# Kernel tuning notes

Hardware: AMD Instinct MI355X
Metric: run time of the kernel (lower is better)

Reference implementation:

```python
import jax, jax.numpy as jnp
import numpy as np

NUM_HEADS = 8
IN_CH = 512
SCALING = float(IN_CH // 8) ** (-0.5)  # 0.125, as in the torch module


def _conv1x1(x, w, b):
    # x: [B,C,H,W], w: [O,C], b: [O]  (1x1 conv == channel matmul)
    return jnp.einsum('bchw,oc->bohw', x, w) + b[None, :, None, None]


def setup_inputs() -> dict:
    key = jax.random.key(0)
    ks = jax.random.split(key, 9)
    B, C, H, W = 4, IN_CH, 96, 96
    q = jax.random.normal(ks[0], (B, C, H, W), jnp.float32)
    v = jax.random.normal(ks[1], (B, C, H, W), jnp.float32)
    # xavier_uniform for [C,C] 1x1 conv weights
    limit = float(np.sqrt(6.0 / (C + C)))
    Wq = jax.random.uniform(ks[2], (C, C), jnp.float32, -limit, limit)
    Wk = jax.random.uniform(ks[3], (C, C), jnp.float32, -limit, limit)
    Wv = jax.random.uniform(ks[4], (C, C), jnp.float32, -limit, limit)
    bq = jnp.zeros((C,), jnp.float32)
    bk = jnp.zeros((C,), jnp.float32)
    bv = jnp.zeros((C,), jnp.float32)
    # gamma is init to 0 in the module; use a nonzero value so the output is nontrivial
    gamma = jax.random.normal(ks[5], (1,), jnp.float32) * 0.1
    return {'q': q, 'v': v, 'Wq': Wq, 'bq': bq, 'Wk': Wk, 'bk': bk,
            'Wv': Wv, 'bv': bv, 'gamma': gamma}


def reference(q, v, Wq, bq, Wk, bk, Wv, bv, gamma):
    B, C, H, W = q.shape
    nh = NUM_HEADS
    hd = C // nh
    t = _conv1x1(q, Wq, bq) * SCALING           # proj_query
    f = _conv1x1(q, Wk, bk)                     # proj_key
    g = _conv1x1(v, Wv, bv)                     # proj_value
    t = t.reshape(B * nh, hd, H, W)
    f = f.reshape(B * nh, hd, H, W)
    g = g.reshape(B * nh, hd, H, W)
    # criss-cross affinity: row (same y, all x') and column (same x, all y'!=y)
    e_row = jnp.einsum('bdyx,bdyi->byxi', t, f)  # [Bh, H, W, W]
    e_col = jnp.einsum('bdyx,bdix->byxi', t, f)  # [Bh, H, W, H]
    # exclude the current position from the column branch (CUDA kernel skips i==y)
    diag = (jnp.arange(H)[:, None, None] == jnp.arange(H)[None, None, :])  # [H,1,H]
    e_col = jnp.where(diag, -jnp.inf, e_col)
    attn = jax.nn.softmax(jnp.concatenate([e_row, e_col], axis=-1), axis=-1)  # [Bh,H,W,W+H]
    a_row, a_col = attn[..., :W], attn[..., W:]
    out = (jnp.einsum('byxi,bdyi->bdyx', a_row, g)
           + jnp.einsum('byxi,bdix->bdyx', a_col, g))  # [Bh, hd, H, W]
    out = out.reshape(B, C, H, W)
    return gamma[0] * out + v
```

## Files before the change

kernel.cpp:

```cpp
#include <hip/hip_runtime.h>
#include <hip/hip_bf16.h>

typedef __bf16 bf16;
typedef __attribute__((ext_vector_type(8))) __bf16 bf16x8;
typedef __attribute__((ext_vector_type(4))) float floatx4;

#define B_  4
#define C_  512
#define H_  96
#define W_  96
#define HD_ 64
#define HW_ 9216
#define BH_ 32
#define SCALING_ 0.125f
#define BHS_ 589824

static constexpr size_t T_ELEMS = (size_t)BH_ * HD_ * HW_;
static constexpr size_t S_ELEMS = (size_t)BH_ * HW_;

__global__ __launch_bounds__(256) void cast_w(
    const float* __restrict__ Wq, const float* __restrict__ Wk, const float* __restrict__ Wv,
    bf16* __restrict__ Wb)
{
    const int i  = blockIdx.x * 256 + threadIdx.x;
    const int e0 = i * 4;
    const int arr = e0 >> 18;
    const int off = e0 & 262143;
    const float* W = (arr == 0) ? Wq : (arr == 1) ? Wk : Wv;
    const float4 val = *(const float4*)(W + off);
    bf16 tmp[4] __attribute__((aligned(8)));
    tmp[0] = (bf16)val.x; tmp[1] = (bf16)val.y; tmp[2] = (bf16)val.z; tmp[3] = (bf16)val.w;
    *(uint2*)(Wb + e0) = *(const uint2*)tmp;
}

__global__ __launch_bounds__(256) void cast_qv(
    const float* __restrict__ q, const float* __restrict__ v,
    bf16* __restrict__ qbT, bf16* __restrict__ vbT)
{
    const int z = blockIdx.z;
    const int s = z >> 2, b = z & 3;
    const float* sb = (s ? v : q) + (size_t)b * C_ * HW_;
    bf16*       db = (s ? vbT : qbT) + (size_t)b * HW_ * C_;
    const int p0 = blockIdx.x * 64, c0 = blockIdx.y * 64;

    __shared__ float ts[64][65];
    const int tid = threadIdx.x;

    for (int i = tid; i < 1024; i += 256) {
        const int row = i >> 4, seg = i & 15;
        const float4 val = *(const float4*)(sb + (size_t)(c0 + row) * HW_ + p0 + seg * 4);
        ts[row][seg * 4 + 0] = val.x; ts[row][seg * 4 + 1] = val.y;
        ts[row][seg * 4 + 2] = val.z; ts[row][seg * 4 + 3] = val.w;
    }
    __syncthreads();
    for (int i = tid; i < 512; i += 256) {
        const int prow = i >> 3, cseg = i & 7;
        bf16 tmp[8] __attribute__((aligned(16)));
        #pragma unroll
        for (int k = 0; k < 8; k++) tmp[k] = (bf16)ts[cseg * 8 + k][prow];
        *(uint4*)(db + (size_t)(p0 + prow) * C_ + c0 + cseg * 8) = *(const uint4*)tmp;
    }
}

__device__ __forceinline__ void stage_swz(
    const bf16* __restrict__ A, const bf16* __restrict__ Bsrc,
    int o0, int p0, int k0, int tid, bf16* As, bf16* Bs)
{
    #pragma unroll
    for (int c = tid; c < 512; c += 256) {
        const int sc = c ^ ((c >> 3) & 7);
        const int row = sc >> 2, seg = sc & 3;
        const bf16* gA = A    + (size_t)(o0 + row) * C_ + k0 + seg * 8;
        const bf16* gB = Bsrc + (size_t)(p0 + row) * C_ + k0 + seg * 8;
#if __has_builtin(__builtin_amdgcn_global_load_lds)
        char* lA = (char*)As + (size_t)(c & ~63) * 16;
        char* lB = (char*)Bs + (size_t)(c & ~63) * 16;
        __builtin_amdgcn_global_load_lds((const __attribute__((address_space(1))) void*)gA,
                                         (__attribute__((address_space(3))) void*)lA, 16, 0, 0);
        __builtin_amdgcn_global_load_lds((const __attribute__((address_space(1))) void*)gB,
                                         (__attribute__((address_space(3))) void*)lB, 16, 0, 0);
#else
        *(uint4*)((char*)As + (size_t)c * 16) = *(const uint4*)gA;
        *(uint4*)((char*)Bs + (size_t)c * 16) = *(const uint4*)gB;
#endif
    }
}

__device__ __forceinline__ void stage3_swz(
    const bf16* __restrict__ A0, const bf16* __restrict__ A1, const bf16* __restrict__ Bsrc,
    int o0, int p0, int k0, int tid, bf16* As0, bf16* As1, bf16* Bs)
{
    #pragma unroll
    for (int c = tid; c < 512; c += 256) {
        const int sc = c ^ ((c >> 3) & 7);
        const int row = sc >> 2, seg = sc & 3;
        const bf16* gA0 = A0   + (size_t)(o0 + row) * C_ + k0 + seg * 8;
        const bf16* gA1 = A1   + (size_t)(o0 + row) * C_ + k0 + seg * 8;
        const bf16* gB  = Bsrc + (size_t)(p0 + row) * C_ + k0 + seg * 8;
#if __has_builtin(__builtin_amdgcn_global_load_lds)
        char* lA0 = (char*)As0 + (size_t)(c & ~63) * 16;
        char* lA1 = (char*)As1 + (size_t)(c & ~63) * 16;
        char* lB  = (char*)Bs  + (size_t)(c & ~63) * 16;
        __builtin_amdgcn_global_load_lds((const __attribute__((address_space(1))) void*)gA0,
                                         (__attribute__((address_space(3))) void*)lA0, 16, 0, 0);
        __builtin_amdgcn_global_load_lds((const __attribute__((address_space(1))) void*)gA1,
                                         (__attribute__((address_space(3))) void*)lA1, 16, 0, 0);
        __builtin_amdgcn_global_load_lds((const __attribute__((address_space(1))) void*)gB,
                                         (__attribute__((address_space(3))) void*)lB, 16, 0, 0);
#else
        *(uint4*)((char*)As0 + (size_t)c * 16) = *(const uint4*)gA0;
        *(uint4*)((char*)As1 + (size_t)c * 16) = *(const uint4*)gA1;
        *(uint4*)((char*)Bs  + (size_t)c * 16) = *(const uint4*)gB;
#endif
    }
}

__device__ __forceinline__ int swz_chunk(int r, int quad)
{
    return (r * 4 + quad) ^ ((r >> 1) & 7);
}

__device__ __forceinline__ void compute_swz(
    const bf16* As, const bf16* Bs,
    int mrow, int ncol, int l16, int quad, floatx4 acc[4][4])
{
    bf16x8 af[4], bf_[4];
    #pragma unroll
    for (int i = 0; i < 4; i++)
        af[i] = *(const bf16x8*)&As[swz_chunk(mrow + i * 16 + l16, quad) * 8];
    #pragma unroll
    for (int j = 0; j < 4; j++)
        bf_[j] = *(const bf16x8*)&Bs[swz_chunk(ncol + j * 16 + l16, quad) * 8];
    #pragma unroll
    for (int i = 0; i < 4; i++)
        #pragma unroll
        for (int j = 0; j < 4; j++)
            acc[i][j] = __builtin_amdgcn_mfma_f32_16x16x32_bf16(af[i], bf_[j], acc[i][j], 0, 0, 0);
}

__device__ __forceinline__ void compute2_swz(
    const bf16* As0, const bf16* As1, const bf16* Bs,
    int mrow, int ncol, int l16, int quad, floatx4 acc0[4][4], floatx4 acc1[4][4])
{
    bf16x8 a0[4], a1[4], bb[4];
    #pragma unroll
    for (int i = 0; i < 4; i++) {
        const int pc = swz_chunk(mrow + i * 16 + l16, quad);
        a0[i] = *(const bf16x8*)&As0[pc * 8];
        a1[i] = *(const bf16x8*)&As1[pc * 8];
    }
    #pragma unroll
    for (int j = 0; j < 4; j++)
        bb[j] = *(const bf16x8*)&Bs[swz_chunk(ncol + j * 16 + l16, quad) * 8];
    #pragma unroll
    for (int i = 0; i < 4; i++)
        #pragma unroll
        for (int j = 0; j < 4; j++)
            acc0[i][j] = __builtin_amdgcn_mfma_f32_16x16x32_bf16(a0[i], bb[j], acc0[i][j], 0, 0, 0);
    #pragma unroll
    for (int i = 0; i < 4; i++)
        #pragma unroll
        for (int j = 0; j < 4; j++)
            acc1[i][j] = __builtin_amdgcn_mfma_f32_16x16x32_bf16(a1[i], bb[j], acc1[i][j], 0, 0, 0);
}

__global__ __launch_bounds__(256, 2) void conv_qk(
    const bf16* __restrict__ Wb,
    const float* __restrict__ bq, const float* __restrict__ bk,
    const bf16* __restrict__ qbT,
    bf16* __restrict__ tR, bf16* __restrict__ fR)
{
    const int b = blockIdx.z;
    const bf16* A0   = Wb;
    const bf16* A1   = Wb + (size_t)C_ * C_;
    const bf16* Bsrc = qbT + (size_t)b * HW_ * C_;

    const int p0 = blockIdx.x * 128;
    const int o0 = blockIdx.y * 128;

    __shared__ __align__(16) bf16 smem[24576];
    bf16* const As0_0 = smem;
    bf16* const As1_0 = smem + 4096;
    bf16* const Bs_0  = smem + 8192;
    bf16* const As0_1 = smem + 12288;
    bf16* const As1_1 = smem + 16384;
    bf16* const Bs_1  = smem + 20480;

    const int tid = threadIdx.x, lane = tid & 63;
    const int wave = tid >> 6, l16 = lane & 15, quad = lane >> 4;
    const int mrow = (wave >> 1) * 64, ncol = (wave & 1) * 64;

    floatx4 acc0[4][4] = {};
    floatx4 acc1[4][4] = {};

    stage3_swz(A0, A1, Bsrc, o0, p0, 0, tid, As0_0, As1_0, Bs_0);
    __syncthreads();

    for (int k0 = 0; k0 < C_; k0 += 64) {
        if (k0 + 32 < C_) stage3_swz(A0, A1, Bsrc, o0, p0, k0 + 32, tid, As0_1, As1_1, Bs_1);
        compute2_swz(As0_0, As1_0, Bs_0, mrow, ncol, l16, quad, acc0, acc1);
        __syncthreads();
        if (k0 + 64 < C_) stage3_swz(A0, A1, Bsrc, o0, p0, k0 + 64, tid, As0_0, As1_0, Bs_0);
        compute2_swz(As0_1, As1_1, Bs_1, mrow, ncol, l16, quad, acc0, acc1);
        __syncthreads();
    }

    auto epi = [&](floatx4 (&ac)[4][4], const float* __restrict__ bias,
                   float scale, bf16* __restrict__ dst) {
        #pragma unroll
        for (int i = 0; i < 4; i++)
            #pragma unroll
            for (int r = 0; r < 4; r++) {
                const int ol_ = mrow + i * 16 + quad * 4 + r;
                const float bi = bias[o0 + ol_];
                #pragma unroll
                for (int j = 0; j < 4; j++) {
                    const int pl = ncol + j * 16 + l16;
                    smem[pl * 128 + (ol_ ^ ((pl & 7) << 3))] = (bf16)((ac[i][j][r] + bi) * scale);
                }
            }
        __syncthreads();
        #pragma unroll
        for (int c = tid; c < 2048; c += 256) {
            const int pl = c >> 4, oo = c & 15;
            const int pg = p0 + pl;
            const int y = pg / 96, x = pg - y * 96;
            const int og = o0 + oo * 8;
            const int bh = b * 8 + (og >> 6), d = og & 63;
            const size_t di = (size_t)bh * BHS_ + (size_t)y * 6144 + x * 64 + d;
            *(uint4*)(dst + di) = *(const uint4*)&smem[pl * 128 + ((oo ^ (pl & 7)) * 8)];
        }
    };
    epi(acc0, bq, SCALING_, tR);
    __syncthreads();
    epi(acc1, bk, 1.0f, fR);
}

__global__ __launch_bounds__(256) void conv_v(
    const bf16* __restrict__ Wb,
    const float* __restrict__ bv,
    const bf16* __restrict__ vbT,
    bf16* __restrict__ g)
{
    const int b = blockIdx.z;
    const bf16* A    = Wb + (size_t)2 * C_ * C_;
    const bf16* Bsrc = vbT + (size_t)b * HW_ * C_;

    const int p0 = blockIdx.x * 128;
    const int o0 = blockIdx.y * 128;

    __shared__ __align__(16) bf16 smem[17408];
    bf16* const As0 = smem;
    bf16* const Bs0 = smem + 4096;
    bf16* const As1 = smem + 8192;
    bf16* const Bs1 = smem + 12288;

    const int tid = threadIdx.x, lane = tid & 63;
    const int wave = tid >> 6, l16 = lane & 15, quad = lane >> 4;
    const int mrow = (wave >> 1) * 64, ncol = (wave & 1) * 64;

    floatx4 acc[4][4] = {};

    stage_swz(A, Bsrc, o0, p0, 0, tid, As0, Bs0);
    __syncthreads();

    for (int k0 = 0; k0 < C_; k0 += 64) {
        if (k0 + 32 < C_) stage_swz(A, Bsrc, o0, p0, k0 + 32, tid, As1, Bs1);
        compute_swz(As0, Bs0, mrow, ncol, l16, quad, acc);
        __syncthreads();
        if (k0 + 64 < C_) stage_swz(A, Bsrc, o0, p0, k0 + 64, tid, As0, Bs0);
        compute_swz(As1, Bs1, mrow, ncol, l16, quad, acc);
        __syncthreads();
    }

    const int TS = 136;
    #pragma unroll
    for (int i = 0; i < 4; i++)
        #pragma unroll
        for (int r = 0; r < 4; r++) {
            const int ol_ = mrow + i * 16 + quad * 4 + r;
            const float bi = bv[o0 + ol_];
            #pragma unroll
            for (int j = 0; j < 4; j++) {
                const int pl = ncol + j * 16 + l16;
                smem[ol_ * TS + pl] = (bf16)(acc[i][j][r] + bi);
            }
        }
    __syncthreads();
    #pragma unroll
    for (int c = tid; c < 2048; c += 256) {
        const int ol_ = c >> 4, po = c & 15;
        const size_t di = (size_t)(b * 512 + o0 + ol_) * HW_ + p0 + po * 8;
        *(uint4*)(g + di) = *(const uint4*)&smem[ol_ * TS + po * 8];
    }
}

__global__ __launch_bounds__(256) void transpose_g(const bf16* __restrict__ src, bf16* __restrict__ dst)
{
    const int plane = blockIdx.y;
    const int y0 = blockIdx.x * 32;
    const bf16* s = src + (size_t)plane * HW_;
    bf16*       d = dst + (size_t)plane * HW_;

    __shared__ bf16 ts[32][100];
    const int tid = threadIdx.x;

    #pragma unroll
    for (int i = tid; i < 768; i += 256) {
        const int row = i / 24, seg = i % 24;
        *(uint2*)&ts[row][seg * 4] = *(const uint2*)(s + (size_t)(y0 + row) * W_ + seg * 4);
    }
    __syncthreads();
    #pragma unroll
    for (int i = tid; i < 768; i += 256) {
        const int x = i >> 3, yseg = i & 7;
        bf16 tmp[4] __attribute__((aligned(8)));
        #pragma unroll
        for (int k = 0; k < 4; k++) tmp[k] = ts[yseg * 4 + k][x];
        *(uint2*)(d + (size_t)x * H_ + y0 + yseg * 4) = *(const uint2*)tmp;
    }
}

__global__ __launch_bounds__(512) void attn_col(
    const bf16* __restrict__ tR, const bf16* __restrict__ fR, const bf16* __restrict__ gT,
    bf16* __restrict__ outC, float* __restrict__ mc, float* __restrict__ lc)
{
    const int x = blockIdx.x;
    const int bh = blockIdx.y;

    __shared__ __align__(16) bf16 tl[96][72];
    __shared__ __align__(16) bf16 fl[96][72];
    __shared__ __align__(16) bf16 gl[64][104];
    __shared__ __align__(16) bf16 el[96][104];

    const int tid = threadIdx.x;
    const size_t sbase = (size_t)bh * BHS_;

    for (int i = tid; i < 768; i += 512) {
        const int y = i >> 3, oct = i & 7;
        const size_t gi = sbase + (size_t)y * 6144 + (size_t)x * 64 + oct * 8;
        *(uint4*)&tl[y][oct * 8] = *(const uint4*)(tR + gi);
        *(uint4*)&fl[y][oct * 8] = *(const uint4*)(fR + gi);
    }
    const size_t gbase = sbase + (size_t)x * 96;
    for (int i = tid; i < 768; i += 512) {
        const int d = i / 12, seg = i % 12;
        *(uint4*)&gl[d][seg * 8] = *(const uint4*)(gT + gbase + (size_t)d * HW_ + seg * 8);
    }
    __syncthreads();

    const int lane = tid & 63, wave = tid >> 6;
    const int l16 = lane & 15, quad = lane >> 4;

    #pragma unroll
    for (int it = 0; it < 5; it++) {
        const int idx = wave + it * 8;
        if (idx < 36) {
            const int mt = idx / 6, nt = idx % 6;
            floatx4 a = {};
            #pragma unroll
            for (int ks = 0; ks < 2; ks++) {
                bf16x8 af = *(const bf16x8*)&tl[mt * 16 + l16][ks * 32 + quad * 8];
                bf16x8 bf_ = *(const bf16x8*)&fl[nt * 16 + l16][ks * 32 + quad * 8];
                a = __builtin_amdgcn_mfma_f32_16x16x32_bf16(af, bf_, a, 0, 0, 0);
            }
            #pragma unroll
            for (int r = 0; r < 4; r++) {
                const int row = mt * 16 + quad * 4 + r, col = nt * 16 + l16;
                el[row][col] = (row == col) ? (bf16)(-1e30f) : (bf16)a[r];
            }
        }
    }
    __syncthreads();

    if (tid < 384) {
        const int r = tid >> 2, qu = tid & 3;
        float vals[24];
        float m = -1e30f;
        #pragma unroll
        for (int k = 0; k < 3; k++) {
            bf16x8 v8 = *(const bf16x8*)&el[r][qu * 24 + k * 8];
            #pragma unroll
            for (int e = 0; e < 8; e++) { vals[k * 8 + e] = (float)v8[e]; m = fmaxf(m, vals[k * 8 + e]); }
        }
        m = fmaxf(m, __shfl_xor(m, 1));
        m = fmaxf(m, __shfl_xor(m, 2));
        float s = 0.f;
        #pragma unroll
        for (int k = 0; k < 3; k++) {
            bf16 tmp[8] __attribute__((aligned(16)));
            #pragma unroll
            for (int e = 0; e < 8; e++) {
                const float p = __expf(vals[k * 8 + e] - m);
                s += p; tmp[e] = (bf16)p;
            }
            *(uint4*)&el[r][qu * 24 + k * 8] = *(const uint4*)tmp;
        }
        s += __shfl_xor(s, 1);
        s += __shfl_xor(s, 2);
        if (qu == 0) {
            mc[(size_t)bh * HW_ + x * 96 + r] = m;
            lc[(size_t)bh * HW_ + x * 96 + r] = s;
        }
    }
    __syncthreads();

    bf16 (*ol)[72] = tl;
    #pragma unroll
    for (int it = 0; it < 3; it++) {
        const int idx = wave + it * 8;
        const int mt = idx >> 2, nt = idx & 3;
        floatx4 a = {};
        #pragma unroll
        for (int ks = 0; ks < 3; ks++) {
            bf16x8 pf = *(const bf16x8*)&el[mt * 16 + l16][ks * 32 + quad * 8];
            bf16x8 gf = *(const bf16x8*)&gl[nt * 16 + l16][ks * 32 + quad * 8];
            a = __builtin_amdgcn_mfma_f32_16x16x32_bf16(pf, gf, a, 0, 0, 0);
        }
        #pragma unroll
        for (int r = 0; r < 4; r++)
            ol[mt * 16 + quad * 4 + r][nt * 16 + l16] = (bf16)a[r];
    }
    __syncthreads();

    bf16* ob = outC + sbase + (size_t)x * 6144;
    for (int i = tid; i < 768; i += 512) {
        const int j = i >> 3, oct = i & 7;
        *(uint4*)(ob + (size_t)j * 64 + oct * 8) = *(const uint4*)&ol[j][oct * 8];
    }
}

__global__ __launch_bounds__(512) void attn_row_merge(
    const bf16* __restrict__ tR, const bf16* __restrict__ fR, const bf16* __restrict__ g,
    const bf16* __restrict__ outC, const float* __restrict__ mc, const float* __restrict__ lc,
    const float* __restrict__ v, const float* __restrict__ gamma, float* __restrict__ out)
{
    const int y = blockIdx.x;
    const int bh = blockIdx.y;

    __shared__ __align__(16) bf16 tl[96][72];
    __shared__ __align__(16) bf16 fl[96][72];
    __shared__ __align__(16) bf16 gl[64][104];
    __shared__ __align__(16) bf16 el[96][104];
    __shared__ float mll[96], lll[96], wrl[96], wcl[96];

    const int tid = threadIdx.x;
    const size_t sbase = (size_t)bh * BHS_;
    const size_t slice = sbase + (size_t)y * 6144;

    for (int i = tid; i < 768; i += 512) {
        const int j = i >> 3, oct = i & 7;
        *(uint4*)&tl[j][oct * 8] = *(const uint4*)(tR + slice + (size_t)j * 64 + oct * 8);
        *(uint4*)&fl[j][oct * 8] = *(const uint4*)(fR + slice + (size_t)j * 64 + oct * 8);
    }
    const size_t gbase = sbase + (size_t)y * 96;
    for (int i = tid; i < 768; i += 512) {
        const int d = i / 12, seg = i % 12;
        *(uint4*)&gl[d][seg * 8] = *(const uint4*)(g + gbase + (size_t)d * HW_ + seg * 8);
    }
    __syncthreads();

    const int lane = tid & 63, wave = tid >> 6;
    const int l16 = lane & 15, quad = lane >> 4;

    #pragma unroll
    for (int it = 0; it < 5; it++) {
        const int idx = wave + it * 8;
        if (idx < 36) {
            const int mt = idx / 6, nt = idx % 6;
            floatx4 a = {};
            #pragma unroll
            for (int ks = 0; ks < 2; ks++) {
                bf16x8 af = *(const bf16x8*)&tl[mt * 16 + l16][ks * 32 + quad * 8];
                bf16x8 bf_ = *(const bf16x8*)&fl[nt * 16 + l16][ks * 32 + quad * 8];
                a = __builtin_amdgcn_mfma_f32_16x16x32_bf16(af, bf_, a, 0, 0, 0);
            }
            #pragma unroll
            for (int r = 0; r < 4; r++)
                el[mt * 16 + quad * 4 + r][nt * 16 + l16] = (bf16)a[r];
        }
    }
    __syncthreads();

    if (tid < 384) {
        const int r = tid >> 2, qu = tid & 3;
        float vals[24];
        float m = -1e30f;
        #pragma unroll
        for (int k = 0; k < 3; k++) {
            bf16x8 v8 = *(const bf16x8*)&el[r][qu * 24 + k * 8];
            #pragma unroll
            for (int e = 0; e < 8; e++) { vals[k * 8 + e] = (float)v8[e]; m = fmaxf(m, vals[k * 8 + e]); }
        }
        m = fmaxf(m, __shfl_xor(m, 1));
        m = fmaxf(m, __shfl_xor(m, 2));
        float s = 0.f;
        #pragma unroll
        for (int k = 0; k < 3; k++) {
            bf16 tmp[8] __attribute__((aligned(16)));
            #pragma unroll
            for (int e = 0; e < 8; e++) {
                const float p = __expf(vals[k * 8 + e] - m);
                s += p; tmp[e] = (bf16)p;
            }
            *(uint4*)&el[r][qu * 24 + k * 8] = *(const uint4*)tmp;
        }
        s += __shfl_xor(s, 1);
        s += __shfl_xor(s, 2);
        if (qu == 0) { mll[r] = m; lll[r] = s; }
    }
    __syncthreads();

    if (tid < 96) {
        const float mrv = mll[tid], lrv = lll[tid];
        const float mcv = mc[(size_t)bh * HW_ + tid * 96 + y];
        const float lcv = lc[(size_t)bh * HW_ + tid * 96 + y];
        const float mm = fmaxf(mrv, mcv);
        const float wr = __expf(mrv - mm), wc = __expf(mcv - mm);
        const float dn = lrv * wr + lcv * wc;
        wrl[tid] = wr / dn;
        wcl[tid] = wc / dn;
    }
    bf16 (*ocl)[72] = fl;
    for (int i = tid; i < 768; i += 512) {
        const int xx = i >> 3, oct = i & 7;
        *(uint4*)&ocl[xx][oct * 8] =
            *(const uint4*)(outC + sbase + (size_t)xx * 6144 + (size_t)y * 64 + oct * 8);
    }
    bf16 (*ol)[72] = tl;
    #pragma unroll
    for (int it = 0; it < 3; it++) {
        const int idx = wave + it * 8;
        const int mt = idx >> 2, nt = idx & 3;
        floatx4 a = {};
        #pragma unroll
        for (int ks = 0; ks < 3; ks++) {
            bf16x8 pf = *(const bf16x8*)&el[mt * 16 + l16][ks * 32 + quad * 8];
            bf16x8 gf = *(const bf16x8*)&gl[nt * 16 + l16][ks * 32 + quad * 8];
            a = __builtin_amdgcn_mfma_f32_16x16x32_bf16(pf, gf, a, 0, 0, 0);
        }
        #pragma unroll
        for (int r = 0; r < 4; r++)
            ol[mt * 16 + quad * 4 + r][nt * 16 + l16] = (bf16)a[r];
    }
    __syncthreads();

    const float gam = gamma[0];
    for (int i = tid; i < 768; i += 512) {
        const int xo = i >> 6, d = i & 63;
        const int x0 = xo * 8;
        float res[8];
        #pragma unroll
        for (int k = 0; k < 8; k++) {
            const int xx = x0 + k;
            res[k] = (float)ol[xx][d] * wrl[xx] + (float)ocl[xx][d] * wcl[xx];
        }
        const size_t ob = sbase + (size_t)d * HW_ + (size_t)y * 96 + x0;
        const float4 v0 = *(const float4*)(v + ob);
        const float4 v1 = *(const float4*)(v + ob + 4);
        float4 r0, r1;
        r0.x = gam * res[0] + v0.x; r0.y = gam * res[1] + v0.y;
        r0.z = gam * res[2] + v0.z; r0.w = gam * res[3] + v0.w;
        r1.x = gam * res[4] + v1.x; r1.y = gam * res[5] + v1.y;
        r1.z = gam * res[6] + v1.z; r1.w = gam * res[7] + v1.w;
        *(float4*)(out + ob) = r0;
        *(float4*)(out + ob + 4) = r1;
    }
}

extern "C" void kernel_launch(void* const* d_in, const int* in_sizes, int n_in,
                              void* d_out, int out_size, void* d_ws, size_t ws_size,
                              hipStream_t stream)
{
    const float* q     = (const float*)d_in[0];
    const float* v     = (const float*)d_in[1];
    const float* Wq    = (const float*)d_in[2];
    const float* bq    = (const float*)d_in[3];
    const float* Wk    = (const float*)d_in[4];
    const float* bk    = (const float*)d_in[5];
    const float* Wv    = (const float*)d_in[6];
    const float* bv    = (const float*)d_in[7];
    const float* gamma = (const float*)d_in[8];
    float* out = (float*)d_out;

    char* w = (char*)d_ws;
    const size_t Tb = T_ELEMS * sizeof(bf16);
    bf16* qbT  = (bf16*)(w + 0 * Tb);
    bf16* vbT  = (bf16*)(w + 1 * Tb);
    bf16* tR   = (bf16*)(w + 2 * Tb);
    bf16* fR   = (bf16*)(w + 3 * Tb);
    bf16* g    = (bf16*)(w + 4 * Tb);
    bf16* gT   = (bf16*)(w + 1 * Tb);
    bf16* outC = (bf16*)(w + 0 * Tb);
    bf16* Wb   = (bf16*)(w + 6 * Tb);
    float* mc  = (float*)(w + 6 * Tb + 1572864);
    float* lc  = mc + S_ELEMS;

    cast_w  <<<dim3(768), 256, 0, stream>>>(Wq, Wk, Wv, Wb);
    cast_qv <<<dim3(144, 8, 8), 256, 0, stream>>>(q, v, qbT, vbT);
    conv_v  <<<dim3(72, 4, 4), 256, 0, stream>>>(Wb, bv, vbT, g);
    conv_qk <<<dim3(72, 4, 4), 256, 0, stream>>>(Wb, bq, bk, qbT, tR, fR);
    transpose_g<<<dim3(3, 2048), 256, 0, stream>>>(g, gT);
    attn_col<<<dim3(96, BH_), 512, 0, stream>>>(tR, fR, gT, outC, mc, lc);
    attn_row_merge<<<dim3(96, BH_), 512, 0, stream>>>(tR, fR, g, outC, mc, lc, v, gamma, out);
}
```

Measured before the change: 416.8 us.

## Merge V and QK projections into one launch, prefetch merge inputs, raise MFMA priority

Replaces the separate conv_v and conv_qk launches with one conv_fused grid whose z dimension selects the QK or V projection. This removes a launch and lets the two GEMMs share the device concurrently. In attn_row_merge, the column partial outputs, the residual v values and the column softmax stats are loaded before the row-attention MFMA loop so their global latency overlaps compute. s_setprio is raised around the MFMA loops in both attention kernels. The fused kernel now holds the larger shared-memory footprint and launch bound for the V path too, and the prefetched values raise register pressure.

New measurement: 404.2 us. 3.0% less time.

```diff
diff --git a/kernel.cpp b/kernel.cpp
--- a/kernel.cpp
+++ b/kernel.cpp
@@ -164,134 +164,122 @@
             acc1[i][j] = __builtin_amdgcn_mfma_f32_16x16x32_bf16(a1[i], bb[j], acc1[i][j], 0, 0, 0);
 }
 
-__global__ __launch_bounds__(256, 2) void conv_qk(
+__global__ __launch_bounds__(256, 2) void conv_fused(
     const bf16* __restrict__ Wb,
-    const float* __restrict__ bq, const float* __restrict__ bk,
-    const bf16* __restrict__ qbT,
-    bf16* __restrict__ tR, bf16* __restrict__ fR)
-{
-    const int b = blockIdx.z;
-    const bf16* A0   = Wb;
-    const bf16* A1   = Wb + (size_t)C_ * C_;
-    const bf16* Bsrc = qbT + (size_t)b * HW_ * C_;
-
+    const float* __restrict__ bq, const float* __restrict__ bk, const float* __restrict__ bv,
+    const bf16* __restrict__ qbT, const bf16* __restrict__ vbT,
+    bf16* __restrict__ tR, bf16* __restrict__ fR, bf16* __restrict__ g)
+{
+    __shared__ __align__(16) bf16 smem[24576];
+
+    const int z = blockIdx.z;
     const int p0 = blockIdx.x * 128;
     const int o0 = blockIdx.y * 128;
-
-    __shared__ __align__(16) bf16 smem[24576];
-    bf16* const As0_0 = smem;
-    bf16* const As1_0 = smem + 4096;
-    bf16* const Bs_0  = smem + 8192;
-    bf16* const As0_1 = smem + 12288;
-    bf16* const As1_1 = smem + 16384;
-    bf16* const Bs_1  = smem + 20480;
-
     const int tid = threadIdx.x, lane = tid & 63;
     const int wave = tid >> 6, l16 = lane & 15, quad = lane >> 4;
     const int mrow = (wave >> 1) * 64, ncol = (wave & 1) * 64;
 
-    floatx4 acc0[4][4] = {};
-    floatx4 acc1[4][4] = {};
-
-    stage3_swz(A0, A1, Bsrc, o0, p0, 0, tid, As0_0, As1_0, Bs_0);
-    __syncthreads();
-
-    for (int k0 = 0; k0 < C_; k0 += 64) {
-        if (k0 + 32 < C_) stage3_swz(A0, A1, Bsrc, o0, p0, k0 + 32, tid, As0_1, As1_1, Bs_1);
-        compute2_swz(As0_0, As1_0, Bs_0, mrow, ncol, l16, quad, acc0, acc1);
+    if (z < 4) {
+        const int b = z;
+        const bf16* A0   = Wb;
+        const bf16* A1   = Wb + (size_t)C_ * C_;
+        const bf16* Bsrc = qbT + (size_t)b * HW_ * C_;
+
+        bf16* const As0_0 = smem;
+        bf16* const As1_0 = smem + 4096;
+        bf16* const Bs_0  = smem + 8192;
+        bf16* const As0_1 = smem + 12288;
+        bf16* const As1_1 = smem + 16384;
+        bf16* const Bs_1  = smem + 20480;
+
+        floatx4 acc0[4][4] = {};
+        floatx4 acc1[4][4] = {};
+
+        stage3_swz(A0, A1, Bsrc, o0, p0, 0, tid, As0_0, As1_0, Bs_0);
         __syncthreads();
-        if (k0 + 64 < C_) stage3_swz(A0, A1, Bsrc, o0, p0, k0 + 64, tid, As0_0, As1_0, Bs_0);
-        compute2_swz(As0_1, As1_1, Bs_1, mrow, ncol, l16, quad, acc0, acc1);
+
+        for (int k0 = 0; k0 < C_; k0 += 64) {
+            if (k0 + 32 < C_) stage3_swz(A0, A1, Bsrc, o0, p0, k0 + 32, tid, As0_1, As1_1, Bs_1);
+            compute2_swz(As0_0, As1_0, Bs_0, mrow, ncol, l16, quad, acc0, acc1);
+            __syncthreads();
+            if (k0 + 64 < C_) stage3_swz(A0, A1, Bsrc, o0, p0, k0 + 64, tid, As0_0, As1_0, Bs_0);
+            compute2_swz(As0_1, As1_1, Bs_1, mrow, ncol, l16, quad, acc0, acc1);
+            __syncthreads();
+        }
+
+        auto epi = [&](floatx4 (&ac)[4][4], const float* __restrict__ bias,
+                       float scale, bf16* __restrict__ dst) {
+            #pragma unroll
+            for (int i = 0; i < 4; i++)
+                #pragma unroll
+                for (int r = 0; r < 4; r++) {
+                    const int ol_ = mrow + i * 16 + quad * 4 + r;
+                    const float bi = bias[o0 + ol_];
+                    #pragma unroll
+                    for (int j = 0; j < 4; j++) {
+                        const int pl = ncol + j * 16 + l16;
+                        smem[pl * 128 + (ol_ ^ ((pl & 7) << 3))] = (bf16)((ac[i][j][r] + bi) * scale);
+                    }
+                }
+            __syncthreads();
+            #pragma unroll
+            for (int c = tid; c < 2048; c += 256) {
+                const int pl = c >> 4, oo = c & 15;
+                const int pg = p0 + pl;
+                const int y = pg / 96, x = pg - y * 96;
+                const int og = o0 + oo * 8;
+                const int bh = b * 8 + (og >> 6), d = og & 63;
+                const size_t di = (size_t)bh * BHS_ + (size_t)y * 6144 + x * 64 + d;
+                *(uint4*)(dst + di) = *(const uint4*)&smem[pl * 128 + ((oo ^ (pl & 7)) * 8)];
+            }
+        };
+        epi(acc0, bq, SCALING_, tR);
         __syncthreads();
-    }
-
-    auto epi = [&](floatx4 (&ac)[4][4], const float* __restrict__ bias,
-                   float scale, bf16* __restrict__ dst) {
+        epi(acc1, bk, 1.0f, fR);
+    } else {
+        const int b = z - 4;
+        const bf16* A    = Wb + (size_t)2 * C_ * C_;
+        const bf16* Bsrc = vbT + (size_t)b * HW_ * C_;
+
+        bf16* const As0 = smem;
+        bf16* const Bs0 = smem + 4096;
+        bf16* const As1 = smem + 8192;
+        bf16* const Bs1 = smem + 12288;
+
+        floatx4 acc[4][4] = {};
+
+        stage_swz(A, Bsrc, o0, p0, 0, tid, As0, Bs0);
+        __syncthreads();
+
+        for (int k0 = 0; k0 < C_; k0 += 64) {
+            if (k0 + 32 < C_) stage_swz(A, Bsrc, o0, p0, k0 + 32, tid, As1, Bs1);
+            compute_swz(As0, Bs0, mrow, ncol, l16, quad, acc);
+            __syncthreads();
+            if (k0 + 64 < C_) stage_swz(A, Bsrc, o0, p0, k0 + 64, tid, As0, Bs0);
+            compute_swz(As1, Bs1, mrow, ncol, l16, quad, acc);
+            __syncthreads();
+        }
+
+        const int TS = 136;
         #pragma unroll
         for (int i = 0; i < 4; i++)
             #pragma unroll
             for (int r = 0; r < 4; r++) {
                 const int ol_ = mrow + i * 16 + quad * 4 + r;
-                const float bi = bias[o0 + ol_];
+                const float bi = bv[o0 + ol_];
                 #pragma unroll
                 for (int j = 0; j < 4; j++) {
                     const int pl = ncol + j * 16 + l16;
-                    smem[pl * 128 + (ol_ ^ ((pl & 7) << 3))] = (bf16)((ac[i][j][r] + bi) * scale);
+                    smem[ol_ * TS + pl] = (bf16)(acc[i][j][r] + bi);
                 }
             }
         __syncthreads();
         #pragma unroll
         for (int c = tid; c < 2048; c += 256) {
-            const int pl = c >> 4, oo = c & 15;
-            const int pg = p0 + pl;
-            const int y = pg / 96, x = pg - y * 96;
-            const int og = o0 + oo * 8;
-            const int bh = b * 8 + (og >> 6), d = og & 63;
-            const size_t di = (size_t)bh * BHS_ + (size_t)y * 6144 + x * 64 + d;
-            *(uint4*)(dst + di) = *(const uint4*)&smem[pl * 128 + ((oo ^ (pl & 7)) * 8)];
-        }
-    };
-    epi(acc0, bq, SCALING_, tR);
-    __syncthreads();
-    epi(acc1, bk, 1.0f, fR);
-}
-
-__global__ __launch_bounds__(256) void conv_v(
-    const bf16* __restrict__ Wb,
-    const float* __restrict__ bv,
-    const bf16* __restrict__ vbT,
-    bf16* __restrict__ g)
-{
-    const int b = blockIdx.z;
-    const bf16* A    = Wb + (size_t)2 * C_ * C_;
-    const bf16* Bsrc = vbT + (size_t)b * HW_ * C_;
-
-    const int p0 = blockIdx.x * 128;
-    const int o0 = blockIdx.y * 128;
-
-    __shared__ __align__(16) bf16 smem[17408];
-    bf16* const As0 = smem;
-    bf16* const Bs0 = smem + 4096;
-    bf16* const As1 = smem + 8192;
-    bf16* const Bs1 = smem + 12288;
-
-    const int tid = threadIdx.x, lane = tid & 63;
-    const int wave = tid >> 6, l16 = lane & 15, quad = lane >> 4;
-    const int mrow = (wave >> 1) * 64, ncol = (wave & 1) * 64;
-
-    floatx4 acc[4][4] = {};
-
-    stage_swz(A, Bsrc, o0, p0, 0, tid, As0, Bs0);
-    __syncthreads();
-
-    for (int k0 = 0; k0 < C_; k0 += 64) {
-        if (k0 + 32 < C_) stage_swz(A, Bsrc, o0, p0, k0 + 32, tid, As1, Bs1);
-        compute_swz(As0, Bs0, mrow, ncol, l16, quad, acc);
-        __syncthreads();
-        if (k0 + 64 < C_) stage_swz(A, Bsrc, o0, p0, k0 + 64, tid, As0, Bs0);
-        compute_swz(As1, Bs1, mrow, ncol, l16, quad, acc);
-        __syncthreads();
-    }
-
-    const int TS = 136;
-    #pragma unroll
-    for (int i = 0; i < 4; i++)
-        #pragma unroll
-        for (int r = 0; r < 4; r++) {
-            const int ol_ = mrow + i * 16 + quad * 4 + r;
-            const float bi = bv[o0 + ol_];
-            #pragma unroll
-            for (int j = 0; j < 4; j++) {
-                const int pl = ncol + j * 16 + l16;
-                smem[ol_ * TS + pl] = (bf16)(acc[i][j][r] + bi);
-            }
-        }
-    __syncthreads();
-    #pragma unroll
-    for (int c = tid; c < 2048; c += 256) {
-        const int ol_ = c >> 4, po = c & 15;
-        const size_t di = (size_t)(b * 512 + o0 + ol_) * HW_ + p0 + po * 8;
-        *(uint4*)(g + di) = *(const uint4*)&smem[ol_ * TS + po * 8];
+            const int ol_ = c >> 4, po = c & 15;
+            const size_t di = (size_t)(b * 512 + o0 + ol_) * HW_ + p0 + po * 8;
+            *(uint4*)(g + di) = *(const uint4*)&smem[ol_ * TS + po * 8];
+        }
     }
 }
 
@@ -352,6 +340,7 @@
     const int lane = tid & 63, wave = tid >> 6;
     const int l16 = lane & 15, quad = lane >> 4;
 
+    __builtin_amdgcn_s_setprio(1);
     #pragma unroll
     for (int it = 0; it < 5; it++) {
         const int idx = wave + it * 8;
@@ -371,6 +360,7 @@
             }
         }
     }
+    __builtin_amdgcn_s_setprio(0);
     __syncthreads();
 
     if (tid < 384) {
@@ -406,6 +396,7 @@
     __syncthreads();
 
     bf16 (*ol)[72] = tl;
+    __builtin_amdgcn_s_setprio(1);
     #pragma unroll
     for (int it = 0; it < 3; it++) {
         const int idx = wave + it * 8;
@@ -421,6 +412,7 @@
         for (int r = 0; r < 4; r++)
             ol[mt * 16 + quad * 4 + r][nt * 16 + l16] = (bf16)a[r];
     }
+    __builtin_amdgcn_s_setprio(0);
     __syncthreads();
 
     bf16* ob = outC + sbase + (size_t)x * 6144;
@@ -458,11 +450,40 @@
         const int d = i / 12, seg = i % 12;
         *(uint4*)&gl[d][seg * 8] = *(const uint4*)(g + gbase + (size_t)d * HW_ + seg * 8);
     }
+
+    uint4 oc0, oc1 = {};
+    {
+        const int xx = tid >> 3, oct = tid & 7;
+        oc0 = *(const uint4*)(outC + sbase + (size_t)xx * 6144 + (size_t)y * 64 + oct * 8);
+    }
+    if (tid < 256) {
+        const int i1 = tid + 512, xx = i1 >> 3, oct = i1 & 7;
+        oc1 = *(const uint4*)(outC + sbase + (size_t)xx * 6144 + (size_t)y * 64 + oct * 8);
+    }
+    float4 vp0a, vp0b, vp1a = {}, vp1b = {};
+    {
+        const int xo = tid >> 6, d = tid & 63;
+        const size_t ob = sbase + (size_t)d * HW_ + (size_t)y * 96 + xo * 8;
+        vp0a = *(const float4*)(v + ob);
+        vp0b = *(const float4*)(v + ob + 4);
+    }
+    if (tid < 256) {
+        const int i1 = tid + 512, xo = i1 >> 6, d = i1 & 63;
+        const size_t ob = sbase + (size_t)d * HW_ + (size_t)y * 96 + xo * 8;
+        vp1a = *(const float4*)(v + ob);
+        vp1b = *(const float4*)(v + ob + 4);
+    }
+    float mcv = 0.f, lcv = 0.f;
+    if (tid < 96) {
+        mcv = mc[(size_t)bh * HW_ + tid * 96 + y];
+        lcv = lc[(size_t)bh * HW_ + tid * 96 + y];
+    }
     __syncthreads();
 
     const int lane = tid & 63, wave = tid >> 6;
     const int l16 = lane & 15, quad = lane >> 4;
 
+    __builtin_amdgcn_s_setprio(1);
     #pragma unroll
     for (int it = 0; it < 5; it++) {
         const int idx = wave + it * 8;
@@ -480,7 +501,18 @@
                 el[mt * 16 + quad * 4 + r][nt * 16 + l16] = (bf16)a[r];
         }
     }
-    __syncthreads();
+    __builtin_amdgcn_s_setprio(0);
+    __syncthreads();
+
+    bf16 (*ocl)[72] = fl;
+    {
+        const int xx = tid >> 3, oct = tid & 7;
+        *(uint4*)&ocl[xx][oct * 8] = oc0;
+    }
+    if (tid < 256) {
+        const int i1 = tid + 512, xx = i1 >> 3, oct = i1 & 7;
+        *(uint4*)&ocl[xx][oct * 8] = oc1;
+    }
 
     if (tid < 384) {
         const int r = tid >> 2, qu = tid & 3;
@@ -513,21 +545,14 @@
 
     if (tid < 96) {
         const float mrv = mll[tid], lrv = lll[tid];
-        const float mcv = mc[(size_t)bh * HW_ + tid * 96 + y];
-        const float lcv = lc[(size_t)bh * HW_ + tid * 96 + y];
         const float mm = fmaxf(mrv, mcv);
         const float wr = __expf(mrv - mm), wc = __expf(mcv - mm);
         const float dn = lrv * wr + lcv * wc;
         wrl[tid] = wr / dn;
         wcl[tid] = wc / dn;
     }
-    bf16 (*ocl)[72] = fl;
-    for (int i = tid; i < 768; i += 512) {
-        const int xx = i >> 3, oct = i & 7;
-        *(uint4*)&ocl[xx][oct * 8] =
-            *(const uint4*)(outC + sbase + (size_t)xx * 6144 + (size_t)y * 64 + oct * 8);
-    }
     bf16 (*ol)[72] = tl;
+    __builtin_amdgcn_s_setprio(1);
     #pragma unroll
     for (int it = 0; it < 3; it++) {
         const int idx = wave + it * 8;
@@ -543,11 +568,12 @@
         for (int r = 0; r < 4; r++)
             ol[mt * 16 + quad * 4 + r][nt * 16 + l16] = (bf16)a[r];
     }
+    __builtin_amdgcn_s_setprio(0);
     __syncthreads();
 
     const float gam = gamma[0];
-    for (int i = tid; i < 768; i += 512) {
-        const int xo = i >> 6, d = i & 63;
+    {
+        const int xo = tid >> 6, d = tid & 63;
         const int x0 = xo * 8;
         float res[8];
         #pragma unroll
@@ -556,13 +582,30 @@
             res[k] = (float)ol[xx][d] * wrl[xx] + (float)ocl[xx][d] * wcl[xx];
         }
         const size_t ob = sbase + (size_t)d * HW_ + (size_t)y * 96 + x0;
-        const float4 v0 = *(const float4*)(v + ob);
-        const float4 v1 = *(const float4*)(v + ob + 4);
         float4 r0, r1;
-        r0.x = gam * res[0] + v0.x; r0.y = gam * res[1] + v0.y;
-        r0.z = gam * res[2] + v0.z; r0.w = gam * res[3] + v0.w;
-        r1.x = gam * res[4] + v1.x; r1.y = gam * res[5] + v1.y;
-        r1.z = gam * res[6] + v1.z; r1.w = gam * res[7] + v1.w;
+        r0.x = gam * res[0] + vp0a.x; r0.y = gam * res[1] + vp0a.y;
+        r0.z = gam * res[2] + vp0a.z; r0.w = gam * res[3] + vp0a.w;
+        r1.x = gam * res[4] + vp0b.x; r1.y = gam * res[5] + vp0b.y;
+        r1.z = gam * res[6] + vp0b.z; r1.w = gam * res[7] + vp0b.w;
+        *(float4*)(out + ob) = r0;
+        *(float4*)(out + ob + 4) = r1;
+    }
+    if (tid < 256) {
+        const int i1 = tid + 512;
+        const int xo = i1 >> 6, d = i1 & 63;
+        const int x0 = xo * 8;
+        float res[8];
+        #pragma unroll
+        for (int k = 0; k < 8; k++) {
+            const int xx = x0 + k;
+            res[k] = (float)ol[xx][d] * wrl[xx] + (float)ocl[xx][d] * wcl[xx];
+        }
+        const size_t ob = sbase + (size_t)d * HW_ + (size_t)y * 96 + x0;
+        float4 r0, r1;
+        r0.x = gam * res[0] + vp1a.x; r0.y = gam * res[1] + vp1a.y;
+        r0.z = gam * res[2] + vp1a.z; r0.w = gam * res[3] + vp1a.w;
+        r1.x = gam * res[4] + vp1b.x; r1.y = gam * res[5] + vp1b.y;
+        r1.z = gam * res[6] + vp1b.z; r1.w = gam * res[7] + vp1b.w;
         *(float4*)(out + ob) = r0;
         *(float4*)(out + ob + 4) = r1;
     }
@@ -598,8 +641,7 @@
 
     cast_w  <<<dim3(768), 256, 0, stream>>>(Wq, Wk, Wv, Wb);
     cast_qv <<<dim3(144, 8, 8), 256, 0, stream>>>(q, v, qbT, vbT);
-    conv_v  <<<dim3(72, 4, 4), 256, 0, stream>>>(Wb, bv, vbT, g);
-    conv_qk <<<dim3(72, 4, 4), 256, 0, stream>>>(Wb, bq, bk, qbT, tR, fR);
+    conv_fused<<<dim3(72, 4, 8), 256, 0, stream>>>(Wb, bq, bk, bv, qbT, vbT, tR, fR, g);
     transpose_g<<<dim3(3, 2048), 256, 0, stream>>>(g, gT);
     attn_col<<<dim3(96, BH_), 512, 0, stream>>>(tR, fR, gT, outC, mc, lc);
     attn_row_merge<<<dim3(96, BH_), 512, 0, stream>>>(tR, fR, g, outC, mc, lc, v, gamma, out);
```
